# Kernel tuning notes

Hardware: AMD Instinct MI355X
Metric: run time of the kernel (lower is better)

The kernel has to match this reference:

```python
import jax, jax.numpy as jnp
import numpy as np

B, L, D, N = 2, 2048, 1024, 16
HD = D // N  # head_dim = 64
EPS = 1e-5


def layer_norm(x, gamma, beta):
    mu = jnp.mean(x, axis=-1, keepdims=True)
    var = jnp.mean(jnp.square(x - mu), axis=-1, keepdims=True)
    return (x - mu) * jax.lax.rsqrt(var + EPS) * gamma + beta


def setup_inputs() -> dict:
    key = jax.random.key(0)
    ks = jax.random.split(key, 10)
    s = lambda fan_in: 1.0 / np.sqrt(fan_in)
    return {
        "x": jax.random.normal(ks[0], (B, L, D), dtype=jnp.float32),
        "wq": jax.random.uniform(ks[1], (D, D), jnp.float32, -s(D), s(D)),
        "wk": jax.random.uniform(ks[2], (D, D), jnp.float32, -s(D), s(D)),  # shared w_proj (k and v)
        "wo": jax.random.uniform(ks[3], (D, D), jnp.float32, -s(D), s(D)),
        "g1": jnp.ones((D,), jnp.float32),
        "b1": jnp.zeros((D,), jnp.float32),
        "w1": jax.random.uniform(ks[4], (D, 4 * D), jnp.float32, -s(D), s(D)),
        "bb1": jax.random.uniform(ks[5], (4 * D,), jnp.float32, -s(D), s(D)),
        "w2": jax.random.uniform(ks[6], (4 * D, D), jnp.float32, -s(4 * D), s(4 * D)),
        "bb2": jax.random.uniform(ks[7], (D,), jnp.float32, -s(4 * D), s(4 * D)),
        "g2": jnp.ones((D,), jnp.float32),
        "b2": jnp.zeros((D,), jnp.float32),
    }


def reference(x, wq, wk, wo, g1, b1, w1, bb1, w2, bb2, g2, b2):
    b, l, d = x.shape
    # projections (w_proj is shared for k and v in the source; v output is unused)
    q = (x @ wq).reshape(b, l, HD, N)
    k = (x @ wk).reshape(b, l, HD, N)
    # attention scores [b, l, m, n]; softmax over m (dim=2 in source)
    scores = jnp.einsum('bldn,bmdn->blmn', q, k) / np.sqrt(HD).astype(np.float32)
    attn = jax.nn.softmax(scores, axis=2)
    # NOTE: source contracts attention weights with K, not V (faithful bug reproduction)
    ctx = jnp.einsum('blmn,bmdn->bldn', attn, k).reshape(b, l, d)
    attn_out = ctx @ wo
    # post-LN residual block
    h = layer_norm(x + attn_out, g1, b1)
    ff = jax.nn.gelu(h @ w1 + bb1, approximate=False) @ w2 + bb2
    return layer_norm(h + ff, g2, b2)
```

## Files before the change

### kernel.cpp

```cpp
#include <hip/hip_runtime.h>
#include <math.h>

typedef unsigned short u16;
typedef unsigned int u32;
typedef __bf16 bf16x8 __attribute__((ext_vector_type(8)));
typedef unsigned short us8 __attribute__((ext_vector_type(8)));
typedef unsigned short us4 __attribute__((ext_vector_type(4)));
typedef float f32x4 __attribute__((ext_vector_type(4)));

#define DEV __device__ __forceinline__

DEV float fast_exp2(float x) { return __builtin_amdgcn_exp2f(x); }

DEV u16 f2bf(float f) {
  __bf16 h = (__bf16)f;
  return __builtin_bit_cast(u16, h);
}

DEV bf16x8 ld_bf8(const u16* p) { return __builtin_bit_cast(bf16x8, *(const us8*)p); }

DEV void gload_lds16(const u16* g, u16* l) {
  __builtin_amdgcn_global_load_lds((const __attribute__((address_space(1))) void*)g,
                                   (__attribute__((address_space(3))) void*)l, 16, 0, 0);
}

DEV f32x4 mfma16(bf16x8 a, bf16x8 b, f32x4 c) {
  return __builtin_amdgcn_mfma_f32_16x16x32_bf16(a, b, c, 0, 0, 0);
}


__global__ void conv_bf16_kernel(const float* __restrict__ in, u16* __restrict__ out, int n4) {
  const int stride = gridDim.x * blockDim.x;
  for (int i = blockIdx.x * blockDim.x + threadIdx.x; i < n4; i += stride) {
    float4 v = ((const float4*)in)[i];
    us4 h; h[0] = f2bf(v.x); h[1] = f2bf(v.y); h[2] = f2bf(v.z); h[3] = f2bf(v.w);
    ((us4*)out)[i] = h;
  }
}

template <int P>
__global__ __launch_bounds__(256) void transpose_bf16_kernel(
    const float* __restrict__ in, u16* __restrict__ out, int K, int N, float scale) {
  __shared__ float tile[32][33];
  const int nbk = K >> 5;
  const int bk = blockIdx.x % nbk, bn = blockIdx.x / nbk;
  const int r0 = bk << 5, c0 = bn << 5;
  const int t = threadIdx.x;
  {
    const int r = t >> 3, c4 = (t & 7) << 2;
    int sr = r0 + r;
    if constexpr (P == 2) sr = ((sr & 63) << 4) | (sr >> 6);
    const float4 v = *(const float4*)(in + (size_t)sr * N + c0 + c4);
    tile[r][c4] = v.x; tile[r][c4 + 1] = v.y; tile[r][c4 + 2] = v.z; tile[r][c4 + 3] = v.w;
  }
  __syncthreads();
  {
    const int oc = t >> 3, r4 = (t & 7) << 2;
    int orow = c0 + oc;
    if constexpr (P == 1) orow = ((orow & 15) << 6) | (orow >> 4);
    us4 h;
#pragma unroll
    for (int j = 0; j < 4; j++) h[j] = f2bf(tile[r4 + j][oc] * scale);
    *(us4*)(out + (size_t)orow * K + r0 + r4) = h;
  }
}

__global__ __launch_bounds__(256) void khead_transpose(
    const u16* __restrict__ qk, u16* __restrict__ kth) {
  __shared__ u16 tT[64 * 64];
  char* base = (char*)tT;
  const int t = threadIdx.x;
  const int bid = blockIdx.x;
  const int lt = bid & 31, n = (bid >> 5) & 15, b = bid >> 9;
#pragma unroll
  for (int rr = 0; rr < 2; rr++) {
    const int l = rr * 32 + (t >> 3);
    const int d0 = (t & 7) * 8;
    us8 v = *(const us8*)(qk + ((size_t)(b * 2048 + lt * 64 + l)) * 2048 + 1024 + n * 64 + d0);
#pragma unroll
    for (int j = 0; j < 8; j++) {
      const int d = d0 + j;
      *(u16*)(base + d * 128 + ((2 * l) ^ (16 * (d >> 3)))) = v[j];
    }
  }
  __syncthreads();
  const int w = t >> 6, lane = t & 63;
#pragma unroll
  for (int rr = 0; rr < 2; rr++) {
    const int d = rr * 32 + w * 8 + (lane >> 3);
    const int l = (lane & 7) * 8;
    us8 v = *(const us8*)(base + d * 128 + ((2 * l) ^ (16 * (d >> 3))));
    *(us8*)(kth + ((size_t)((b * 16 + n) * 64 + d)) * 2048 + lt * 64 + l) = v;
  }
}

template <int MODE, int BN, int KS>
__global__ __launch_bounds__(256) void gemm128(
    const u16* __restrict__ A, const u16* __restrict__ BT,
    int M, int N, int K,
    u16* __restrict__ ob, float* __restrict__ of,
    const float* __restrict__ res, const float* __restrict__ bias) {
  constexpr int NJ = BN / 32;
  constexpr int WCC = BN / 2;
  __shared__ u16 As[2][4096];
  __shared__ u16 Bs[2][BN * 32];
  const int t = threadIdx.x;
  const int nbm = M >> 7;
  const int nblk = nbm * (N / BN) * KS;
  int bid = blockIdx.x;
  bid = (bid & 7) * (nblk >> 3) + (bid >> 3);
  int ks = 0;
  if constexpr (KS > 1) { ks = bid % KS; bid /= KS; }
  const int bm = bid % nbm;
  const int bn = bid / nbm;
  const int m0 = bm << 7, n0 = bn * BN;
  const int kbeg = ks * (K / KS);
  const int KB = K / KS;
  const int w = t >> 6, lane = t & 63;
  const int wr = w >> 1, wc = w & 1;
  const int lr = lane & 15, lg = lane >> 4, lq = (lane >> 4) << 2;
  const int rsw = (lg ^ (lr & 3)) << 3;

  const int srow = t >> 2;
  const int sseg = (t & 3) ^ (srow & 3);
  const u16* ap = A + (size_t)(m0 + srow) * K + kbeg + sseg * 8;
  const u16* bp = BT + (size_t)(n0 + srow) * K + kbeg + sseg * 8;
  const size_t half = (size_t)64 * K;

#define STAGE(buf, k0)                                                 \
  {                                                                    \
    gload_lds16(ap + (k0), &As[buf][t << 3]);                          \
    gload_lds16(ap + half + (k0), &As[buf][(t << 3) + 2048]);          \
    gload_lds16(bp + (k0), &Bs[buf][t << 3]);                          \
    if constexpr (BN == 128)                                           \
      gload_lds16(bp + half + (k0), &Bs[buf][(t << 3) + 2048]);        \
  }

  f32x4 acc[4][NJ];
#pragma unroll
  for (int i = 0; i < 4; i++)
#pragma unroll
    for (int j = 0; j < NJ; j++) acc[i][j] = (f32x4){0.f, 0.f, 0.f, 0.f};

  STAGE(0, 0);
  __syncthreads();
  const int NI = KB >> 5;
  for (int it = 0; it < NI; ++it) {
    const int buf = it & 1;
    if (it + 1 < NI) STAGE(buf ^ 1, (it + 1) << 5);
    bf16x8 af[4], bfr[NJ];
#pragma unroll
    for (int i = 0; i < 4; i++)
      af[i] = ld_bf8(&As[buf][(wr * 64 + i * 16 + lr) * 32 + rsw]);
#pragma unroll
    for (int j = 0; j < NJ; j++)
      bfr[j] = ld_bf8(&Bs[buf][(wc * WCC + j * 16 + lr) * 32 + rsw]);
#pragma unroll
    for (int i = 0; i < 4; i++)
#pragma unroll
      for (int j = 0; j < NJ; j++) acc[i][j] = mfma16(af[i], bfr[j], acc[i][j]);
    __syncthreads();
  }
#undef STAGE

#pragma unroll
  for (int i = 0; i < 4; i++) {
    const int r0 = m0 + wr * 64 + i * 16 + lq;
#pragma unroll
    for (int j = 0; j < NJ; j++) {
      const int c = n0 + wc * WCC + j * 16 + lr;
      if constexpr (MODE == 0) {
#pragma unroll
        for (int q = 0; q < 4; q++) ob[(size_t)(r0 + q) * N + c] = f2bf(acc[i][j][q]);
      } else if constexpr (MODE == 2) {
#pragma unroll
        for (int q = 0; q < 4; q++) {
          const size_t idx = (size_t)(r0 + q) * N + c;
          of[idx] = acc[i][j][q] + res[idx];
        }
      } else if constexpr (MODE == 3) {
        const float bv = bias[c];
#pragma unroll
        for (int q = 0; q < 4; q++) {
          float u = acc[i][j][q] + bv;
          float gl = 0.5f * u * (1.f + erff(u * 0.70710678118f));
          ob[(size_t)(r0 + q) * N + c] = f2bf(gl);
        }
      } else {
        const size_t ofs = (size_t)ks * M * N;
#pragma unroll
        for (int q = 0; q < 4; q++) {
          of[ofs + (size_t)(r0 + q) * N + c] = acc[i][j][q];
        }
      }
    }
  }
}

__global__ __launch_bounds__(256, 2) void attn_kernel(
    const u16* __restrict__ qk, const u16* __restrict__ kth, u16* __restrict__ ctxh) {
  __shared__ u16 KsB[2][4096];
  __shared__ u16 KtsB[2][4096];
  __shared__ u16 Plds[4][2048];
  const int t = threadIdx.x, w = t >> 6, lane = t & 63;
  const int lr = lane & 15, lg = lane >> 4;
  int bid = blockIdx.x;
  bid = (bid & 7) * 64 + (bid >> 3);
  const int qb = bid & 15, hn = (bid >> 4) & 15, b = bid >> 8;
  const int lw = qb * 128 + w * 32;
  const u16* ksrc = qk + (size_t)b * 2048 * 2048 + 1024 + hn * 64;
  const u16* ktb = kth + ((size_t)(b * 16 + hn)) * 64 * 2048;
  char* pb = (char*)&Plds[w][0];
  const int swz = (lr & 7) << 4;

#define STAGE_KV(buf, m0s)                                                    \
  {                                                                           \
    _Pragma("unroll") for (int i_ = 0; i_ < 2; i_++) {                        \
      const int s_ = t + 256 * i_;                                            \
      const int row_ = s_ >> 3;                                               \
      const int c_ = (s_ & 7) ^ (row_ & 7);                                   \
      gload_lds16(ksrc + (size_t)((m0s) + row_) * 2048 + c_ * 8,              \
                  &KsB[buf][s_ * 8]);                                         \
      gload_lds16(ktb + (size_t)row_ * 2048 + (m0s) + c_ * 8,                 \
                  &KtsB[buf][s_ * 8]);                                        \
    }                                                                         \
  }

  bf16x8 qf[2][2];
#pragma unroll
  for (int f = 0; f < 2; f++)
#pragma unroll
    for (int kk = 0; kk < 2; kk++)
      qf[f][kk] = ld_bf8(qk + (size_t)(b * 2048 + lw + 16 * f + lr) * 2048 + hn * 64 +
                         kk * 32 + lg * 8);

  float mrow[2] = {-1e30f, -1e30f}, lrow[2] = {0.f, 0.f};
  f32x4 o[2][4];
#pragma unroll
  for (int f = 0; f < 2; f++)
#pragma unroll
    for (int dj = 0; dj < 4; dj++) o[f][dj] = (f32x4){0.f, 0.f, 0.f, 0.f};

  STAGE_KV(0, 0);
  __syncthreads();

  for (int it = 0; it < 32; ++it) {
    const int buf = it & 1;
    if (it < 31) STAGE_KV(buf ^ 1, (it + 1) * 64);

    f32x4 sc[2][4];
#pragma unroll
    for (int f = 0; f < 2; f++)
#pragma unroll
      for (int mj = 0; mj < 4; mj++) sc[f][mj] = (f32x4){0.f, 0.f, 0.f, 0.f};
#pragma unroll
    for (int mj = 0; mj < 4; mj++) {
      const int krow = 16 * mj + lr;
      bf16x8 kf0 = ld_bf8(&KsB[buf][krow * 64 + ((lg ^ (krow & 7)) << 3)]);
      bf16x8 kf1 = ld_bf8(&KsB[buf][krow * 64 + (((4 + lg) ^ (krow & 7)) << 3)]);
#pragma unroll
      for (int f = 0; f < 2; f++) {
        sc[f][mj] = mfma16(kf0, qf[f][0], sc[f][mj]);
        sc[f][mj] = mfma16(kf1, qf[f][1], sc[f][mj]);
      }
    }

#pragma unroll
    for (int f = 0; f < 2; f++) {
      float tm = fmaxf(fmaxf(sc[f][0][0], sc[f][0][1]), fmaxf(sc[f][0][2], sc[f][0][3]));
#pragma unroll
      for (int mj = 1; mj < 4; mj++)
        tm = fmaxf(tm, fmaxf(fmaxf(sc[f][mj][0], sc[f][mj][1]),
                             fmaxf(sc[f][mj][2], sc[f][mj][3])));
      tm = fmaxf(tm, __shfl_xor(tm, 16));
      tm = fmaxf(tm, __shfl_xor(tm, 32));
      if (!__all(tm <= mrow[f] + 8.f)) {
        const float mnew = fmaxf(mrow[f], tm);
        const float al = fast_exp2(mrow[f] - mnew);
        mrow[f] = mnew;
        lrow[f] *= al;
        float albc[4];
#pragma unroll
        for (int q = 0; q < 4; q++) albc[q] = __shfl(al, 4 * lg + q);
#pragma unroll
        for (int dj = 0; dj < 4; dj++)
#pragma unroll
          for (int q = 0; q < 4; q++) o[f][dj][q] *= albc[q];
      }
      float ts = 0.f;
      char* pf = pb + f * 2048;
#pragma unroll
      for (int mj = 0; mj < 4; mj++) {
        float p0 = fast_exp2(sc[f][mj][0] - mrow[f]);
        float p1 = fast_exp2(sc[f][mj][1] - mrow[f]);
        float p2 = fast_exp2(sc[f][mj][2] - mrow[f]);
        float p3 = fast_exp2(sc[f][mj][3] - mrow[f]);
        ts += (p0 + p1) + (p2 + p3);
        u32 w0 = (u32)f2bf(p0) | ((u32)f2bf(p1) << 16);
        u32 w1 = (u32)f2bf(p2) | ((u32)f2bf(p3) << 16);
        *(uint2*)(pf + ((lr * 128 + mj * 32 + lg * 8) ^ swz)) = make_uint2(w0, w1);
      }
      ts += __shfl_xor(ts, 16);
      ts += __shfl_xor(ts, 32);
      lrow[f] += ts;
    }

    bf16x8 pa[2][2];
#pragma unroll
    for (int f = 0; f < 2; f++)
#pragma unroll
      for (int kk = 0; kk < 2; kk++)
        pa[f][kk] = __builtin_bit_cast(
            bf16x8, *(const us8*)(pb + f * 2048 + ((lr * 128 + kk * 64 + lg * 16) ^ swz)));

#pragma unroll
    for (int dj = 0; dj < 4; dj++) {
      const int vrow = dj * 16 + lr;
      bf16x8 v0 = ld_bf8(&KtsB[buf][vrow * 64 + ((lg ^ (vrow & 7)) << 3)]);
      bf16x8 v1 = ld_bf8(&KtsB[buf][vrow * 64 + (((4 + lg) ^ (vrow & 7)) << 3)]);
#pragma unroll
      for (int f = 0; f < 2; f++) {
        o[f][dj] = mfma16(pa[f][0], v0, o[f][dj]);
        o[f][dj] = mfma16(pa[f][1], v1, o[f][dj]);
      }
    }
    __syncthreads();
  }
#undef STAGE_KV

#pragma unroll
  for (int f = 0; f < 2; f++) {
    const float inv = 1.f / lrow[f];
    float invbc[4];
#pragma unroll
    for (int q = 0; q < 4; q++) invbc[q] = __shfl(inv, 4 * lg + q);
#pragma unroll
    for (int q = 0; q < 4; q++) {
      const int ll = lw + 16 * f + 4 * lg + q;
#pragma unroll
      for (int dj = 0; dj < 4; dj++) {
        ctxh[((size_t)(b * 2048 + ll)) * 1024 + hn * 64 + dj * 16 + lr] =
            f2bf(o[f][dj][q] * invbc[q]);
      }
    }
  }
}

template <int V>
__global__ __launch_bounds__(256) void ln_kernel(
    const float* __restrict__ in, const float* __restrict__ in2,
    const float* __restrict__ res, const float* __restrict__ bias,
    const float* __restrict__ gamma, const float* __restrict__ beta,
    float* __restrict__ o32, u16* __restrict__ o16) {
  __shared__ float red[8];
  const int row = blockIdx.x, t = threadIdx.x;
  float4 v = ((const float4*)(in + (size_t)row * 1024))[t];
  if constexpr (V == 1) {
    const float4 v2 = ((const float4*)(in2 + (size_t)row * 1024))[t];
    const float4 vr = ((const float4*)(res + (size_t)row * 1024))[t];
    const float4 vb = ((const float4*)bias)[t];
    v.x += v2.x + vr.x + vb.x;
    v.y += v2.y + vr.y + vb.y;
    v.z += v2.z + vr.z + vb.z;
    v.w += v2.w + vr.w + vb.w;
  }
  float s = v.x + v.y + v.z + v.w;
  float ss = v.x * v.x + v.y * v.y + v.z * v.z + v.w * v.w;
#pragma unroll
  for (int off = 1; off < 64; off <<= 1) {
    s += __shfl_xor(s, off);
    ss += __shfl_xor(ss, off);
  }
  if ((t & 63) == 0) { red[t >> 6] = s; red[4 + (t >> 6)] = ss; }
  __syncthreads();
  const float st = red[0] + red[1] + red[2] + red[3];
  const float sst = red[4] + red[5] + red[6] + red[7];
  const float mean = st * (1.f / 1024.f);
  const float var = sst * (1.f / 1024.f) - mean * mean;
  const float rs = rsqrtf(var + 1e-5f);
  const float4 gv = ((const float4*)gamma)[t];
  const float4 bv = ((const float4*)beta)[t];
  float4 ov;
  ov.x = (v.x - mean) * rs * gv.x + bv.x;
  ov.y = (v.y - mean) * rs * gv.y + bv.y;
  ov.z = (v.z - mean) * rs * gv.z + bv.z;
  ov.w = (v.w - mean) * rs * gv.w + bv.w;
  ((float4*)(o32 + (size_t)row * 1024))[t] = ov;
  if (o16) {
    us4 h;
    h[0] = f2bf(ov.x); h[1] = f2bf(ov.y); h[2] = f2bf(ov.z); h[3] = f2bf(ov.w);
    *(us4*)(o16 + (size_t)row * 1024 + t * 4) = h;
  }
}

extern "C" void kernel_launch(void* const* d_in, const int* in_sizes, int n_in,
                              void* d_out, int out_size, void* d_ws, size_t ws_size,
                              hipStream_t stream) {
  const float* x   = (const float*)d_in[0];
  const float* wq  = (const float*)d_in[1];
  const float* wk  = (const float*)d_in[2];
  const float* wo  = (const float*)d_in[3];
  const float* g1  = (const float*)d_in[4];
  const float* b1  = (const float*)d_in[5];
  const float* w1  = (const float*)d_in[6];
  const float* bb1 = (const float*)d_in[7];
  const float* w2  = (const float*)d_in[8];
  const float* bb2 = (const float*)d_in[9];
  const float* g2  = (const float*)d_in[10];
  const float* b2  = (const float*)d_in[11];

  char* ws = (char*)d_ws;
  const size_t MB = 1ull << 20;
  u16* w2T   = (u16*)(ws + 0 * MB);
  u16* w1T   = (u16*)(ws + 8 * MB);
  u16* woT   = (u16*)(ws + 16 * MB);
  u16* wqkT  = (u16*)(ws + 18 * MB);
  u16* xb    = (u16*)(ws + 22 * MB);
  u16* qk    = (u16*)(ws + 30 * MB);
  u16* kthp  = (u16*)(ws + 46 * MB);
  u16* ctxh  = (u16*)(ws + 54 * MB);
  float* rbuf = (float*)(ws + 62 * MB);
  u16* hb    = (u16*)(ws + 78 * MB);
  float* hbuf = (float*)(ws + 86 * MB);
  u16* tbuf  = (u16*)(ws + 18 * MB);
  float* rA   = (float*)(ws + 50 * MB);

  conv_bf16_kernel<<<1024, 256, 0, stream>>>(x, xb, 1048576);
  transpose_bf16_kernel<1><<<1024, 256, 0, stream>>>(wq, wqkT, 1024, 1024, 0.125f * 1.44269504089f);
  transpose_bf16_kernel<1><<<1024, 256, 0, stream>>>(wk, wqkT + (size_t)1024 * 1024, 1024, 1024, 1.0f);
  transpose_bf16_kernel<2><<<1024, 256, 0, stream>>>(wo, woT, 1024, 1024, 1.0f);
  transpose_bf16_kernel<0><<<32 * 128, 256, 0, stream>>>(w1, w1T, 1024, 4096, 1.0f);
  transpose_bf16_kernel<0><<<128 * 32, 256, 0, stream>>>(w2, w2T, 4096, 1024, 1.0f);

  gemm128<0, 128, 1><<<32 * 16, 256, 0, stream>>>(xb, wqkT, 4096, 2048, 1024, qk, nullptr, nullptr, nullptr);
  khead_transpose<<<1024, 256, 0, stream>>>(qk, kthp);

  attn_kernel<<<512, 256, 0, stream>>>(qk, kthp, ctxh);

  gemm128<2, 64, 1><<<32 * 16, 256, 0, stream>>>(ctxh, woT, 4096, 1024, 1024, nullptr, rbuf, x, nullptr);
  ln_kernel<0><<<4096, 256, 0, stream>>>(rbuf, nullptr, nullptr, nullptr, g1, b1, hbuf, hb);

  gemm128<3, 128, 1><<<32 * 32, 256, 0, stream>>>(hb, w1T, 4096, 4096, 1024, tbuf, nullptr, nullptr, bb1);
  gemm128<5, 128, 2><<<32 * 8 * 2, 256, 0, stream>>>(tbuf, w2T, 4096, 1024, 4096, nullptr, rA, nullptr, nullptr);
  ln_kernel<1><<<4096, 256, 0, stream>>>(rA, rA + (size_t)4096 * 1024, hbuf, bb2, g2, b2, (float*)d_out, nullptr);
}
```

Baseline: 276.4 us.

## Add 256x256 eight-wave GEMM for FFN layers with split-K and bf16 residual

Adds a new 256x256-tile GEMM with 512 threads, 64-deep K steps, double-buffered LDS, manual barrier and waitcnt scheduling, and setprio around MFMA groups. It is used for the FFN up-projection (fused GELU) and the down-projection, which becomes split-K by 4 when the workspace allows. LayerNorm is split into ln1 (bf16 output only) and ln2, which sums the partials and reads the residual from the bf16 copy of h instead of an fp32 buffer. This cuts global traffic and increases data reuse per tile, at the cost of using bf16-rounded residual precision and relying on hand-placed synchronization.

```diff
diff --git a/kernel.cpp b/kernel.cpp
--- a/kernel.cpp
+++ b/kernel.cpp
@@ -16,6 +16,7 @@
   __bf16 h = (__bf16)f;
   return __builtin_bit_cast(u16, h);
 }
+DEV float bf2f(u16 h) { return __builtin_bit_cast(float, (u32)h << 16); }
 
 DEV bf16x8 ld_bf8(const u16* p) { return __builtin_bit_cast(bf16x8, *(const us8*)p); }
 
@@ -27,6 +28,10 @@
 DEV f32x4 mfma16(bf16x8 a, bf16x8 b, f32x4 c) {
   return __builtin_amdgcn_mfma_f32_16x16x32_bf16(a, b, c, 0, 0, 0);
 }
+
+#define BAR __builtin_amdgcn_s_barrier()
+#define LGK asm volatile("s_waitcnt lgkmcnt(0)" ::: "memory")
+#define VM4 asm volatile("s_waitcnt vmcnt(4)" ::: "memory")
 
 
 __global__ void conv_bf16_kernel(const float* __restrict__ in, u16* __restrict__ out, int n4) {
@@ -94,28 +99,23 @@
   }
 }
 
-template <int MODE, int BN, int KS>
+template <int MODE, int BN>
 __global__ __launch_bounds__(256) void gemm128(
     const u16* __restrict__ A, const u16* __restrict__ BT,
     int M, int N, int K,
-    u16* __restrict__ ob, float* __restrict__ of,
-    const float* __restrict__ res, const float* __restrict__ bias) {
+    u16* __restrict__ ob, float* __restrict__ of, const float* __restrict__ res) {
   constexpr int NJ = BN / 32;
   constexpr int WCC = BN / 2;
   __shared__ u16 As[2][4096];
   __shared__ u16 Bs[2][BN * 32];
   const int t = threadIdx.x;
   const int nbm = M >> 7;
-  const int nblk = nbm * (N / BN) * KS;
+  const int nblk = nbm * (N / BN);
   int bid = blockIdx.x;
   bid = (bid & 7) * (nblk >> 3) + (bid >> 3);
-  int ks = 0;
-  if constexpr (KS > 1) { ks = bid % KS; bid /= KS; }
   const int bm = bid % nbm;
   const int bn = bid / nbm;
   const int m0 = bm << 7, n0 = bn * BN;
-  const int kbeg = ks * (K / KS);
-  const int KB = K / KS;
   const int w = t >> 6, lane = t & 63;
   const int wr = w >> 1, wc = w & 1;
   const int lr = lane & 15, lg = lane >> 4, lq = (lane >> 4) << 2;
@@ -123,8 +123,8 @@
 
   const int srow = t >> 2;
   const int sseg = (t & 3) ^ (srow & 3);
-  const u16* ap = A + (size_t)(m0 + srow) * K + kbeg + sseg * 8;
-  const u16* bp = BT + (size_t)(n0 + srow) * K + kbeg + sseg * 8;
+  const u16* ap = A + (size_t)(m0 + srow) * K + sseg * 8;
+  const u16* bp = BT + (size_t)(n0 + srow) * K + sseg * 8;
   const size_t half = (size_t)64 * K;
 
 #define STAGE(buf, k0)                                                 \
@@ -144,7 +144,7 @@
 
   STAGE(0, 0);
   __syncthreads();
-  const int NI = KB >> 5;
+  const int NI = K >> 5;
   for (int it = 0; it < NI; ++it) {
     const int buf = it & 1;
     if (it + 1 < NI) STAGE(buf ^ 1, (it + 1) << 5);
@@ -172,26 +172,128 @@
       if constexpr (MODE == 0) {
 #pragma unroll
         for (int q = 0; q < 4; q++) ob[(size_t)(r0 + q) * N + c] = f2bf(acc[i][j][q]);
-      } else if constexpr (MODE == 2) {
+      } else {
 #pragma unroll
         for (int q = 0; q < 4; q++) {
           const size_t idx = (size_t)(r0 + q) * N + c;
           of[idx] = acc[i][j][q] + res[idx];
         }
-      } else if constexpr (MODE == 3) {
+      }
+    }
+  }
+}
+
+template <int MODE, int KS>
+__global__ __launch_bounds__(512, 2) void gemm256(
+    const u16* __restrict__ A, const u16* __restrict__ BT,
+    int M, int N, int K,
+    u16* __restrict__ ob, float* __restrict__ of, const float* __restrict__ bias) {
+  __shared__ u16 AL[2][2][8192];
+  __shared__ u16 BL[2][2][8192];
+  const int t = threadIdx.x;
+  const int lane = t & 63, wid = t >> 6;
+  const int lr = lane & 15, lg = lane >> 4;
+  const int wm = wid >> 2, wn = wid & 3;
+  const int nbm = M >> 8, nbn = N >> 8;
+  const int nblk = nbm * nbn * KS;
+  int bid = blockIdx.x;
+  bid = (bid & 7) * (nblk >> 3) + (bid >> 3);
+  int ks = 0;
+  if constexpr (KS > 1) { ks = bid % KS; bid /= KS; }
+  const int bm = bid % nbm, bn = bid / nbm;
+  const int m0 = bm << 8, n0 = bn << 8;
+  const int KB = K / KS;
+  const int NT = KB >> 6;
+  const u16* Ag = A + (size_t)m0 * K + ks * KB;
+  const u16* Bg = BT + (size_t)n0 * K + ks * KB;
+  const int sseg = (t & 7) ^ (((t >> 5) & 1) << 1);
+  const int akey = ((lr >> 2) & 1) << 1;
+
+  auto stgA = [&](int buf, int h, int kt) {
+    const u16* s = Ag + (size_t)(h * 128 + (t >> 3)) * K + kt * 64 + sseg * 8;
+    gload_lds16(s, &AL[buf][h][t * 8]);
+    gload_lds16(s + (size_t)64 * K, &AL[buf][h][4096 + t * 8]);
+  };
+  auto stgB = [&](int buf, int h, int kt) {
+    const u16* s = Bg + (size_t)(h * 128 + (t >> 3)) * K + kt * 64 + sseg * 8;
+    gload_lds16(s, &BL[buf][h][t * 8]);
+    gload_lds16(s + (size_t)64 * K, &BL[buf][h][4096 + t * 8]);
+  };
+
+#define RDA(DST, BUF, IB)                                                      \
+  _Pragma("unroll") for (int i4 = 0; i4 < 4; i4++)                             \
+  _Pragma("unroll") for (int kk = 0; kk < 2; kk++)                             \
+    DST[i4][kk] = ld_bf8(&AL[BUF][wm][((IB + i4) * 16 + lr) * 64 +             \
+                                      ((kk * 4 + lg) ^ akey) * 8]);
+#define RDB(DST, BUF, JB)                                                      \
+  _Pragma("unroll") for (int j2 = 0; j2 < 2; j2++)                             \
+  _Pragma("unroll") for (int kk = 0; kk < 2; kk++)                             \
+    DST[j2][kk] = ld_bf8(&BL[BUF][wn >> 1][((wn & 1) * 64 + (JB + j2) * 16 +   \
+                                            lr) * 64 +                         \
+                                           ((kk * 4 + lg) ^ akey) * 8]);
+#define QUAD(AF, BF, IB, JB)                                                   \
+  __builtin_amdgcn_s_setprio(1);                                               \
+  _Pragma("unroll") for (int i4 = 0; i4 < 4; i4++)                             \
+  _Pragma("unroll") for (int j2 = 0; j2 < 2; j2++)                             \
+  _Pragma("unroll") for (int kk = 0; kk < 2; kk++)                             \
+    acc[IB + i4][JB + j2] = mfma16(AF[i4][kk], BF[j2][kk], acc[IB + i4][JB + j2]); \
+  __builtin_amdgcn_s_setprio(0);
+
+  f32x4 acc[8][4];
+#pragma unroll
+  for (int i = 0; i < 8; i++)
+#pragma unroll
+    for (int j = 0; j < 4; j++) acc[i][j] = (f32x4){0.f, 0.f, 0.f, 0.f};
+  bf16x8 a0[4][2], a1[4][2], b0[2][2], b1[2][2];
+
+  stgA(0, 0, 0); stgA(0, 1, 0); stgB(0, 0, 0); stgB(0, 1, 0);
+  stgA(1, 0, 1); stgA(1, 1, 1);
+  VM4;
+  BAR;
+
+  const int NI = NT >> 1;
+  for (int it = 0; it < NI; ++it) {
+    const int kt1 = 2 * it + 1;
+    const int ktA = (2 * it + 2 < NT) ? 2 * it + 2 : NT - 1;
+    const int ktB = (2 * it + 3 < NT) ? 2 * it + 3 : NT - 1;
+    RDA(a0, 0, 0); RDB(b0, 0, 0); stgB(1, 0, kt1);
+    BAR; QUAD(a0, b0, 0, 0); LGK; BAR;
+    RDA(a1, 0, 4); stgB(1, 1, kt1);
+    BAR; QUAD(a1, b0, 4, 0); LGK; BAR;
+    RDB(b1, 0, 2); stgA(0, 0, ktA);
+    BAR; QUAD(a1, b1, 4, 2); LGK; BAR;
+    stgA(0, 1, ktA);
+    BAR; QUAD(a0, b1, 0, 2); LGK; VM4; BAR;
+    RDA(a0, 1, 0); RDB(b0, 1, 0); stgB(0, 0, ktA);
+    BAR; QUAD(a0, b0, 0, 0); LGK; BAR;
+    RDA(a1, 1, 4); stgB(0, 1, ktA);
+    BAR; QUAD(a1, b0, 4, 0); LGK; BAR;
+    RDB(b1, 1, 2); stgA(1, 0, ktB);
+    BAR; QUAD(a1, b1, 4, 2); LGK; BAR;
+    stgA(1, 1, ktB);
+    BAR; QUAD(a0, b1, 0, 2); LGK; VM4; BAR;
+  }
+#undef RDA
+#undef RDB
+#undef QUAD
+
+#pragma unroll
+  for (int i = 0; i < 8; i++) {
+    const int r = m0 + wm * 128 + i * 16 + lg * 4;
+#pragma unroll
+    for (int j = 0; j < 4; j++) {
+      const int c = n0 + wn * 64 + j * 16 + lr;
+      if constexpr (MODE == 0) {
         const float bv = bias[c];
 #pragma unroll
         for (int q = 0; q < 4; q++) {
           float u = acc[i][j][q] + bv;
-          float gl = 0.5f * u * (1.f + erff(u * 0.70710678118f));
-          ob[(size_t)(r0 + q) * N + c] = f2bf(gl);
+          ob[(size_t)(r + q) * N + c] = f2bf(0.5f * u * (1.f + erff(u * 0.70710678118f)));
         }
       } else {
-        const size_t ofs = (size_t)ks * M * N;
-#pragma unroll
-        for (int q = 0; q < 4; q++) {
-          of[ofs + (size_t)(r0 + q) * N + c] = acc[i][j][q];
-        }
+        float* op = of + (size_t)ks * M * N;
+#pragma unroll
+        for (int q = 0; q < 4; q++) op[(size_t)(r + q) * N + c] = acc[i][j][q];
       }
     }
   }
@@ -346,31 +448,59 @@
   }
 }
 
-template <int V>
-__global__ __launch_bounds__(256) void ln_kernel(
-    const float* __restrict__ in, const float* __restrict__ in2,
-    const float* __restrict__ res, const float* __restrict__ bias,
-    const float* __restrict__ gamma, const float* __restrict__ beta,
-    float* __restrict__ o32, u16* __restrict__ o16) {
+__global__ __launch_bounds__(256) void ln1_kernel(
+    const float* __restrict__ in, const float* __restrict__ gamma,
+    const float* __restrict__ beta, u16* __restrict__ o16) {
   __shared__ float red[8];
   const int row = blockIdx.x, t = threadIdx.x;
-  float4 v = ((const float4*)(in + (size_t)row * 1024))[t];
-  if constexpr (V == 1) {
-    const float4 v2 = ((const float4*)(in2 + (size_t)row * 1024))[t];
-    const float4 vr = ((const float4*)(res + (size_t)row * 1024))[t];
-    const float4 vb = ((const float4*)bias)[t];
-    v.x += v2.x + vr.x + vb.x;
-    v.y += v2.y + vr.y + vb.y;
-    v.z += v2.z + vr.z + vb.z;
-    v.w += v2.w + vr.w + vb.w;
-  }
+  const float4 v = ((const float4*)(in + (size_t)row * 1024))[t];
   float s = v.x + v.y + v.z + v.w;
   float ss = v.x * v.x + v.y * v.y + v.z * v.z + v.w * v.w;
 #pragma unroll
-  for (int off = 1; off < 64; off <<= 1) {
-    s += __shfl_xor(s, off);
-    ss += __shfl_xor(ss, off);
-  }
+  for (int off = 1; off < 64; off <<= 1) { s += __shfl_xor(s, off); ss += __shfl_xor(ss, off); }
+  if ((t & 63) == 0) { red[t >> 6] = s; red[4 + (t >> 6)] = ss; }
+  __syncthreads();
+  const float st = red[0] + red[1] + red[2] + red[3];
+  const float sst = red[4] + red[5] + red[6] + red[7];
+  const float mean = st * (1.f / 1024.f);
+  const float var = sst * (1.f / 1024.f) - mean * mean;
+  const float rs = rsqrtf(var + 1e-5f);
+  const float4 gv = ((const float4*)gamma)[t];
+  const float4 bv = ((const float4*)beta)[t];
+  us4 h;
+  h[0] = f2bf((v.x - mean) * rs * gv.x + bv.x);
+  h[1] = f2bf((v.y - mean) * rs * gv.y + bv.y);
+  h[2] = f2bf((v.z - mean) * rs * gv.z + bv.z);
+  h[3] = f2bf((v.w - mean) * rs * gv.w + bv.w);
+  *(us4*)(o16 + (size_t)row * 1024 + t * 4) = h;
+}
+
+template <int NP>
+__global__ __launch_bounds__(256) void ln2_kernel(
+    const float* __restrict__ p, size_t pstride,
+    const u16* __restrict__ resb, const float* __restrict__ bias,
+    const float* __restrict__ gamma, const float* __restrict__ beta,
+    float* __restrict__ o32) {
+  __shared__ float red[8];
+  const int row = blockIdx.x, t = threadIdx.x;
+  float4 v = ((const float4*)(p + (size_t)row * 1024))[t];
+#pragma unroll
+  for (int k = 1; k < NP; k++) {
+    const float4 v2 = ((const float4*)(p + (size_t)k * pstride + (size_t)row * 1024))[t];
+    v.x += v2.x; v.y += v2.y; v.z += v2.z; v.w += v2.w;
+  }
+  {
+    const us4 rb = *(const us4*)(resb + (size_t)row * 1024 + t * 4);
+    const float4 vb = ((const float4*)bias)[t];
+    v.x += bf2f(rb[0]) + vb.x;
+    v.y += bf2f(rb[1]) + vb.y;
+    v.z += bf2f(rb[2]) + vb.z;
+    v.w += bf2f(rb[3]) + vb.w;
+  }
+  float s = v.x + v.y + v.z + v.w;
+  float ss = v.x * v.x + v.y * v.y + v.z * v.z + v.w * v.w;
+#pragma unroll
+  for (int off = 1; off < 64; off <<= 1) { s += __shfl_xor(s, off); ss += __shfl_xor(ss, off); }
   if ((t & 63) == 0) { red[t >> 6] = s; red[4 + (t >> 6)] = ss; }
   __syncthreads();
   const float st = red[0] + red[1] + red[2] + red[3];
@@ -386,11 +516,6 @@
   ov.z = (v.z - mean) * rs * gv.z + bv.z;
   ov.w = (v.w - mean) * rs * gv.w + bv.w;
   ((float4*)(o32 + (size_t)row * 1024))[t] = ov;
-  if (o16) {
-    us4 h;
-    h[0] = f2bf(ov.x); h[1] = f2bf(ov.y); h[2] = f2bf(ov.z); h[3] = f2bf(ov.w);
-    *(us4*)(o16 + (size_t)row * 1024 + t * 4) = h;
-  }
 }
 
 extern "C" void kernel_launch(void* const* d_in, const int* in_sizes, int n_in,
@@ -412,18 +537,19 @@
   char* ws = (char*)d_ws;
   const size_t MB = 1ull << 20;
   u16* w2T   = (u16*)(ws + 0 * MB);
-  u16* w1T   = (u16*)(ws + 8 * MB);
-  u16* woT   = (u16*)(ws + 16 * MB);
-  u16* wqkT  = (u16*)(ws + 18 * MB);
-  u16* xb    = (u16*)(ws + 22 * MB);
-  u16* qk    = (u16*)(ws + 30 * MB);
-  u16* kthp  = (u16*)(ws + 46 * MB);
-  u16* ctxh  = (u16*)(ws + 54 * MB);
-  float* rbuf = (float*)(ws + 62 * MB);
-  u16* hb    = (u16*)(ws + 78 * MB);
-  float* hbuf = (float*)(ws + 86 * MB);
-  u16* tbuf  = (u16*)(ws + 18 * MB);
-  float* rA   = (float*)(ws + 50 * MB);
+  u16* hb    = (u16*)(ws + 8 * MB);
+  u16* tbuf  = (u16*)(ws + 16 * MB);
+  float* rA  = (float*)(ws + 48 * MB);
+  u16* wqkT  = (u16*)(ws + 26 * MB);
+  u16* xb    = (u16*)(ws + 30 * MB);
+  u16* qk    = (u16*)(ws + 38 * MB);
+  u16* kthp  = (u16*)(ws + 54 * MB);
+  u16* ctxh  = (u16*)(ws + 62 * MB);
+  float* rbuf = (float*)(ws + 70 * MB);
+  u16* w1T   = (u16*)(ws + 86 * MB);
+  u16* woT   = (u16*)(ws + 94 * MB);
+
+  const bool ks4 = ws_size >= 112 * MB;
 
   conv_bf16_kernel<<<1024, 256, 0, stream>>>(x, xb, 1048576);
   transpose_bf16_kernel<1><<<1024, 256, 0, stream>>>(wq, wqkT, 1024, 1024, 0.125f * 1.44269504089f);
@@ -432,15 +558,21 @@
   transpose_bf16_kernel<0><<<32 * 128, 256, 0, stream>>>(w1, w1T, 1024, 4096, 1.0f);
   transpose_bf16_kernel<0><<<128 * 32, 256, 0, stream>>>(w2, w2T, 4096, 1024, 1.0f);
 
-  gemm128<0, 128, 1><<<32 * 16, 256, 0, stream>>>(xb, wqkT, 4096, 2048, 1024, qk, nullptr, nullptr, nullptr);
+  gemm128<0, 128><<<32 * 16, 256, 0, stream>>>(xb, wqkT, 4096, 2048, 1024, qk, nullptr, nullptr);
   khead_transpose<<<1024, 256, 0, stream>>>(qk, kthp);
 
   attn_kernel<<<512, 256, 0, stream>>>(qk, kthp, ctxh);
 
-  gemm128<2, 64, 1><<<32 * 16, 256, 0, stream>>>(ctxh, woT, 4096, 1024, 1024, nullptr, rbuf, x, nullptr);
-  ln_kernel<0><<<4096, 256, 0, stream>>>(rbuf, nullptr, nullptr, nullptr, g1, b1, hbuf, hb);
-
-  gemm128<3, 128, 1><<<32 * 32, 256, 0, stream>>>(hb, w1T, 4096, 4096, 1024, tbuf, nullptr, nullptr, bb1);
-  gemm128<5, 128, 2><<<32 * 8 * 2, 256, 0, stream>>>(tbuf, w2T, 4096, 1024, 4096, nullptr, rA, nullptr, nullptr);
-  ln_kernel<1><<<4096, 256, 0, stream>>>(rA, rA + (size_t)4096 * 1024, hbuf, bb2, g2, b2, (float*)d_out, nullptr);
-}
+  gemm128<2, 64><<<32 * 16, 256, 0, stream>>>(ctxh, woT, 4096, 1024, 1024, nullptr, rbuf, x);
+  ln1_kernel<<<4096, 256, 0, stream>>>(rbuf, g1, b1, hb);
+
+  gemm256<0, 1><<<256, 512, 0, stream>>>(hb, w1T, 4096, 4096, 1024, tbuf, nullptr, bb1);
+  const size_t MN = (size_t)4096 * 1024;
+  if (ks4) {
+    gemm256<1, 4><<<256, 512, 0, stream>>>(tbuf, w2T, 4096, 1024, 4096, nullptr, rA, nullptr);
+    ln2_kernel<4><<<4096, 256, 0, stream>>>(rA, MN, hb, bb2, g2, b2, (float*)d_out);
+  } else {
+    gemm256<1, 2><<<128, 512, 0, stream>>>(tbuf, w2T, 4096, 1024, 4096, nullptr, rA, nullptr);
+    ln2_kernel<2><<<4096, 256, 0, stream>>>(rA, MN, hb, bb2, g2, b2, (float*)d_out);
+  }
+}
```

Result: faster. 267.1 us (-3.4%).
